# Performance work log

Hardware: AMD Instinct MI355X
Metric: run time of the kernel (lower is better)

The kernel has to match this reference:

```python
import jax, jax.numpy as jnp
import numpy as np

D_MODEL = 1024
N_HEAD = 16


def setup_inputs() -> dict:
    key = jax.random.key(0)
    ks = jax.random.split(key, 12)
    B, S, D = 4, 2048, D_MODEL
    scale = 1.0 / np.sqrt(D)
    inp = {
        "Q": jax.random.normal(ks[0], (B, S, D), jnp.float32),
        "K": jax.random.normal(ks[1], (B, S, D), jnp.float32),
        "V": jax.random.normal(ks[2], (B, S, D), jnp.float32),
        "Wq": jax.random.normal(ks[3], (D, D), jnp.float32) * scale,
        "bq": jax.random.normal(ks[4], (D,), jnp.float32) * scale,
        "Wk": jax.random.normal(ks[5], (D, D), jnp.float32) * scale,
        "bk": jax.random.normal(ks[6], (D,), jnp.float32) * scale,
        "Wv": jax.random.normal(ks[7], (D, D), jnp.float32) * scale,
        "bv": jax.random.normal(ks[8], (D,), jnp.float32) * scale,
        "Wo": jax.random.normal(ks[9], (D, D), jnp.float32) * scale,
        "bo": jax.random.normal(ks[10], (D,), jnp.float32) * scale,
    }
    return inp


def _split_heads(x, n_head):
    B, S, D = x.shape
    return x.reshape(B, S, n_head, D // n_head).transpose(0, 2, 1, 3)  # [B,H,S,dh]


def reference(Q, K, V, Wq, bq, Wk, bk, Wv, bv, Wo, bo):
    # torch Linear: x @ W.T + b
    q = _split_heads(Q @ Wq.T + bq, N_HEAD)
    k = _split_heads(K @ Wk.T + bk, N_HEAD)
    v = _split_heads(V @ Wv.T + bv, N_HEAD)
    d_k = k.shape[-1]
    score = jnp.einsum('bhqd,bhkd->bhqk', q, k) / jnp.sqrt(jnp.float32(d_k))
    attn = jax.nn.softmax(score, axis=-1)
    out = jnp.einsum('bhqk,bhkd->bhqd', attn, v)  # [B,H,S,dh]
    B, H, S, dh = out.shape
    out = out.transpose(0, 2, 1, 3).reshape(B, S, H * dh)
    return out @ Wo.T + bo
```

## Files before the change

kernel.cpp:

```cpp
#include <hip/hip_runtime.h>
#include <math.h>

#define D_MODEL 1024
#define N_HEAD  16
#define DH      64
#define SEQ     2048
#define BATCH   4
#define BH      (BATCH*N_HEAD)
#define MROWS   (BATCH*SEQ)

typedef __attribute__((ext_vector_type(8)))  short          s16x8;
typedef __attribute__((ext_vector_type(8)))  unsigned short u16x8;
typedef __attribute__((ext_vector_type(4)))  unsigned short u16x4;
typedef __attribute__((ext_vector_type(4)))  float          f32x4;
typedef __attribute__((ext_vector_type(16))) float          f32x16;
typedef __attribute__((ext_vector_type(4)))  unsigned int   u32x4;

#define QSCALE 0.18033688f

__device__ __forceinline__ unsigned short f2bf(float x) {
    unsigned int u = __float_as_uint(x);
    u += 0x7FFFu + ((u >> 16) & 1u);
    return (unsigned short)(u >> 16);
}

__device__ __forceinline__ unsigned int cvtpk_bf16(float lo, float hi) {
    unsigned int r;
    asm("v_cvt_pk_bf16_f32 %0, %1, %2" : "=v"(r) : "v"(lo), "v"(hi));
    return r;
}

__device__ __forceinline__ float exp2_asm(float x) {
    float r;
    asm("v_exp_f32 %0, %1" : "=v"(r) : "v"(x));
    return r;
}

__global__ __launch_bounds__(256) void conv_w4(const float* __restrict__ w0,
                                               const float* __restrict__ w1,
                                               const float* __restrict__ w2,
                                               const float* __restrict__ w3,
                                               unsigned short* __restrict__ o0,
                                               unsigned short* __restrict__ o1,
                                               unsigned short* __restrict__ o2,
                                               unsigned short* __restrict__ o3)
{
    const float* w; unsigned short* o;
    switch (blockIdx.y) {
        case 0:  w = w0; o = o0; break;
        case 1:  w = w1; o = o1; break;
        case 2:  w = w2; o = o2; break;
        default: w = w3; o = o3; break;
    }
    int i = blockIdx.x * 256 + threadIdx.x;
    const float4* p = (const float4*)w + (size_t)i * 2;
    float4 a = p[0], b = p[1];
    u16x8 v;
    v[0] = f2bf(a.x); v[1] = f2bf(a.y); v[2] = f2bf(a.z); v[3] = f2bf(a.w);
    v[4] = f2bf(b.x); v[5] = f2bf(b.y); v[6] = f2bf(b.z); v[7] = f2bf(b.w);
    *((u16x8*)o + i) = v;
}

template<int MODE, bool AF32>
__global__ __launch_bounds__(256) void gemm_bt(const void* __restrict__ Av,
                                               const unsigned short* __restrict__ W,
                                               const float* __restrict__ bias,
                                               unsigned short* __restrict__ outb,
                                               float* __restrict__ outf,
                                               float oscale)
{
    __shared__ short As[128 * 64];
    __shared__ short Bs[128 * 64];
    const int tid = threadIdx.x;
    const int w = tid >> 6, l = tid & 63;
    const int lr = l & 15, lg = l >> 4;
    const int wm = w >> 1, wn = w & 1;
    const int r0 = blockIdx.x * 128, c0 = blockIdx.y * 128;
    const int srow = tid >> 3;
    const int sc8  = tid & 7;

    f32x4 zz = {0.f, 0.f, 0.f, 0.f};
    f32x4 acc[4][4];
    #pragma unroll
    for (int i = 0; i < 4; ++i)
        #pragma unroll
        for (int j = 0; j < 4; ++j) acc[i][j] = zz;

    const unsigned short* Ab = (const unsigned short*)Av;
    const float*          Af = (const float*)Av;

    u16x8 ar[4], br[4];
    float4 arf[4][2];
    #pragma unroll
    for (int p = 0; p < 4; ++p) {
        int row = p * 32 + srow;
        if (AF32) {
            arf[p][0] = *(const float4*)(Af + (size_t)(r0 + row) * 1024 + sc8 * 8);
            arf[p][1] = *(const float4*)(Af + (size_t)(r0 + row) * 1024 + sc8 * 8 + 4);
        } else {
            ar[p] = *(const u16x8*)(Ab + (size_t)(r0 + row) * 1024 + sc8 * 8);
        }
        br[p] = *(const u16x8*)(W + (size_t)(c0 + row) * 1024 + sc8 * 8);
    }

    for (int ks = 0; ks < 16; ++ks) {
        __syncthreads();
        #pragma unroll
        for (int p = 0; p < 4; ++p) {
            int row = p * 32 + srow;
            if (AF32) {
                u32x4 wd;
                wd[0] = cvtpk_bf16(arf[p][0].x, arf[p][0].y);
                wd[1] = cvtpk_bf16(arf[p][0].z, arf[p][0].w);
                wd[2] = cvtpk_bf16(arf[p][1].x, arf[p][1].y);
                wd[3] = cvtpk_bf16(arf[p][1].z, arf[p][1].w);
                *(u16x8*)&As[row * 64 + ((sc8 ^ (row & 7)) * 8)] = __builtin_bit_cast(u16x8, wd);
            } else {
                *(u16x8*)&As[row * 64 + ((sc8 ^ (row & 7)) * 8)] = ar[p];
            }
            *(u16x8*)&Bs[row * 64 + ((sc8 ^ (row & 7)) * 8)] = br[p];
        }
        __syncthreads();
        if (ks < 15) {
            int k0 = (ks + 1) * 64;
            #pragma unroll
            for (int p = 0; p < 4; ++p) {
                int row = p * 32 + srow;
                if (AF32) {
                    arf[p][0] = *(const float4*)(Af + (size_t)(r0 + row) * 1024 + k0 + sc8 * 8);
                    arf[p][1] = *(const float4*)(Af + (size_t)(r0 + row) * 1024 + k0 + sc8 * 8 + 4);
                } else {
                    ar[p] = *(const u16x8*)(Ab + (size_t)(r0 + row) * 1024 + k0 + sc8 * 8);
                }
                br[p] = *(const u16x8*)(W + (size_t)(c0 + row) * 1024 + k0 + sc8 * 8);
            }
        }
        #pragma unroll
        for (int t = 0; t < 2; ++t) {
            const int k8 = lg + 4 * t;
            s16x8 af[4], bw[4];
            #pragma unroll
            for (int i = 0; i < 4; ++i) {
                int rowa = wm * 64 + i * 16 + lr;
                af[i] = *(const s16x8*)&As[rowa * 64 + ((k8 ^ (rowa & 7)) * 8)];
                int rowb = wn * 64 + i * 16 + lr;
                bw[i] = *(const s16x8*)&Bs[rowb * 64 + ((k8 ^ (rowb & 7)) * 8)];
            }
            #pragma unroll
            for (int i = 0; i < 4; ++i)
                #pragma unroll
                for (int j = 0; j < 4; ++j)
                    acc[i][j] = __builtin_amdgcn_mfma_f32_16x16x32_bf16(af[i], bw[j], acc[i][j], 0, 0, 0);
        }
    }

    #pragma unroll
    for (int i = 0; i < 4; ++i) {
        #pragma unroll
        for (int j = 0; j < 4; ++j) {
            const int colb = c0 + wn * 64 + j * 16 + lr;
            const float bv = bias[colb];
            if (MODE == 2) {
                const int row = r0 + wm * 64 + i * 16 + lg * 4;
                const int b = row >> 11, s = row & 2047;
                const int h = colb >> 6, d = colb & 63;
                u16x4 pv;
                pv[0] = f2bf((acc[i][j][0] + bv) * oscale);
                pv[1] = f2bf((acc[i][j][1] + bv) * oscale);
                pv[2] = f2bf((acc[i][j][2] + bv) * oscale);
                pv[3] = f2bf((acc[i][j][3] + bv) * oscale);
                *(u16x4*)(outb + ((size_t)(b * N_HEAD + h) * DH + d) * SEQ + s) = pv;
            } else {
                #pragma unroll
                for (int rg = 0; rg < 4; ++rg) {
                    const int row = r0 + wm * 64 + i * 16 + lg * 4 + rg;
                    const float v = acc[i][j][rg] + bv;
                    if (MODE == 0) {
                        outf[(size_t)row * D_MODEL + colb] = v;
                    } else {
                        const int b = row >> 11, s = row & 2047;
                        const int h = colb >> 6, d = colb & 63;
                        outb[((size_t)(b * N_HEAD + h) * SEQ + s) * DH + d] = f2bf(v * oscale);
                    }
                }
            }
        }
    }
}

__global__ __launch_bounds__(256) void flash_attn_mfma32(const unsigned short* __restrict__ qb,
                                                         const unsigned short* __restrict__ kb,
                                                         const unsigned short* __restrict__ vtb,
                                                         unsigned short* __restrict__ aob)
{
    __shared__ u16x8 Kt[512];
    __shared__ u16x8 Vt[512];

    const int tid = threadIdx.x;
    const int w = tid >> 6, l = tid & 63;
    const int q32 = l & 31;
    const int h = l >> 5;
    const int qt = blockIdx.x, bh = blockIdx.y;
    const unsigned short* qh = qb + (size_t)bh * SEQ * DH;
    const unsigned short* kh = kb + (size_t)bh * SEQ * DH;
    const unsigned short* vh = vtb + (size_t)bh * DH * SEQ;

    const int qrow = qt * 128 + w * 32 + q32;

    s16x8 qf[4];
    #pragma unroll
    for (int ks = 0; ks < 4; ++ks)
        qf[ks] = *(const s16x8*)(qh + (size_t)qrow * DH + ks * 16 + h * 8);

    f32x16 O[2];
    #pragma unroll
    for (int c = 0; c < 2; ++c)
        #pragma unroll
        for (int r = 0; r < 16; ++r) O[c][r] = 0.f;
    float m = -1e30f, lsum = 0.f;

    const int srow = tid >> 3;
    const int sc8  = tid & 7;

    u16x8 kreg[2], vreg[2];
    #pragma unroll
    for (int p = 0; p < 2; ++p) {
        int rr = p * 32 + srow;
        kreg[p] = *(const u16x8*)(kh + (size_t)rr * DH + sc8 * 8);
        vreg[p] = *(const u16x8*)(vh + (size_t)rr * SEQ + sc8 * 8);
    }

    for (int kv = 0; kv < SEQ / 64; ++kv) {
        __syncthreads();
        #pragma unroll
        for (int p = 0; p < 2; ++p) {
            int rr = p * 32 + srow;
            Kt[sc8 * 64 + (rr ^ sc8)] = kreg[p];
            Vt[sc8 * 64 + (rr ^ sc8)] = vreg[p];
        }
        __syncthreads();
        if (kv < SEQ / 64 - 1) {
            const int s0 = (kv + 1) * 64;
            #pragma unroll
            for (int p = 0; p < 2; ++p) {
                int rr = p * 32 + srow;
                kreg[p] = *(const u16x8*)(kh + (size_t)(s0 + rr) * DH + sc8 * 8);
                vreg[p] = *(const u16x8*)(vh + (size_t)rr * SEQ + s0 + sc8 * 8);
            }
        }

        f32x16 SC[2];
        #pragma unroll
        for (int c = 0; c < 2; ++c)
            #pragma unroll
            for (int r = 0; r < 16; ++r) SC[c][r] = 0.f;
        #pragma unroll
        for (int ks = 0; ks < 4; ++ks) {
            const int chunk = 2 * ks + h;
            #pragma unroll
            for (int c = 0; c < 2; ++c) {
                const int row = c * 32 + q32;
                s16x8 kf = __builtin_bit_cast(s16x8, Kt[chunk * 64 + (row ^ chunk)]);
                SC[c] = __builtin_amdgcn_mfma_f32_32x32x16_bf16(kf, qf[ks], SC[c], 0, 0, 0);
            }
        }

        float t0[8];
        #pragma unroll
        for (int r = 0; r < 8; ++r)
            t0[r] = fmaxf(fmaxf(SC[0][r], SC[0][r + 8]), fmaxf(SC[1][r], SC[1][r + 8]));
        #pragma unroll
        for (int d = 4; d; d >>= 1)
            #pragma unroll
            for (int r = 0; r < d; ++r) t0[r] = fmaxf(t0[r], t0[r + d]);
        float rm = fmaxf(t0[0], __shfl_xor(t0[0], 32, 64));

        if (!__all(rm - m <= 8.0f)) {
            const float nm = fmaxf(m, rm);
            const float fold = exp2_asm(m - nm);
            lsum *= fold;
            O[0] *= fold;
            O[1] *= fold;
            m = nm;
        }

        #pragma unroll
        for (int c = 0; c < 2; ++c)
            #pragma unroll
            for (int r = 0; r < 16; ++r)
                SC[c][r] = exp2_asm(SC[c][r] - m);

        float s0a[8];
        #pragma unroll
        for (int r = 0; r < 8; ++r)
            s0a[r] = (SC[0][r] + SC[0][r + 8]) + (SC[1][r] + SC[1][r + 8]);
        #pragma unroll
        for (int d = 4; d; d >>= 1)
            #pragma unroll
            for (int r = 0; r < d; ++r) s0a[r] += s0a[r + d];
        lsum += s0a[0] + __shfl_xor(s0a[0], 32, 64);

        s16x8 pa[4];
        #pragma unroll
        for (int s = 0; s < 4; ++s) {
            const int c = s >> 1, rb = (s & 1) * 8;
            unsigned int a0 = cvtpk_bf16(SC[c][rb + 0], SC[c][rb + 1]);
            unsigned int a1 = cvtpk_bf16(SC[c][rb + 2], SC[c][rb + 3]);
            unsigned int b0 = cvtpk_bf16(SC[c][rb + 4], SC[c][rb + 5]);
            unsigned int b1 = cvtpk_bf16(SC[c][rb + 6], SC[c][rb + 7]);
            unsigned int x0 = (unsigned int)__shfl_xor((int)a0, 32, 64);
            unsigned int x1 = (unsigned int)__shfl_xor((int)a1, 32, 64);
            unsigned int y0 = (unsigned int)__shfl_xor((int)b0, 32, 64);
            unsigned int y1 = (unsigned int)__shfl_xor((int)b1, 32, 64);
            u32x4 wd;
            wd[0] = h ? y0 : a0;
            wd[1] = h ? y1 : a1;
            wd[2] = h ? b0 : x0;
            wd[3] = h ? b1 : x1;
            pa[s] = __builtin_bit_cast(s16x8, wd);
        }

        #pragma unroll
        for (int s = 0; s < 4; ++s) {
            const int chunk = 2 * s + h;
            #pragma unroll
            for (int c = 0; c < 2; ++c) {
                const int row = c * 32 + q32;
                s16x8 vf = __builtin_bit_cast(s16x8, Vt[chunk * 64 + (row ^ chunk)]);
                O[c] = __builtin_amdgcn_mfma_f32_32x32x16_bf16(vf, pa[s], O[c], 0, 0, 0);
            }
        }
    }

    const float inv = 1.0f / lsum;
    const int b = bh >> 4, head = bh & 15;
    unsigned short* obase = aob + ((size_t)b * SEQ + qrow) * D_MODEL + head * DH;
    #pragma unroll
    for (int c = 0; c < 2; ++c) {
        #pragma unroll
        for (int rq = 0; rq < 4; ++rq) {
            const int d0 = 8 * rq + 4 * h + 32 * c;
            u16x4 pv;
            #pragma unroll
            for (int j = 0; j < 4; ++j) pv[j] = f2bf(O[c][rq * 4 + j] * inv);
            *(u16x4*)(obase + d0) = pv;
        }
    }
}

extern "C" void kernel_launch(void* const* d_in, const int* in_sizes, int n_in,
                              void* d_out, int out_size, void* d_ws, size_t ws_size,
                              hipStream_t stream)
{
    const float* Q  = (const float*)d_in[0];
    const float* K  = (const float*)d_in[1];
    const float* V  = (const float*)d_in[2];
    const float* Wq = (const float*)d_in[3];
    const float* bq = (const float*)d_in[4];
    const float* Wk = (const float*)d_in[5];
    const float* bk = (const float*)d_in[6];
    const float* Wv = (const float*)d_in[7];
    const float* bv = (const float*)d_in[8];
    const float* Wo = (const float*)d_in[9];
    const float* bo = (const float*)d_in[10];

    const size_t PER = (size_t)MROWS * D_MODEL;
    const size_t WSZ = (size_t)D_MODEL * D_MODEL;
    unsigned short* wqb = (unsigned short*)d_ws;
    unsigned short* wkb = wqb + WSZ;
    unsigned short* wvb = wkb + WSZ;
    unsigned short* wob = wvb + WSZ;
    unsigned short* qb2 = wob + WSZ;
    unsigned short* kb2 = qb2 + PER;
    unsigned short* vtb = kb2 + PER;
    unsigned short* aob = vtb + PER;

    dim3 gg(MROWS / 128, D_MODEL / 128);

    conv_w4<<<dim3(512, 4), 256, 0, stream>>>(Wq, Wk, Wv, Wo, wqb, wkb, wvb, wob);

    gemm_bt<1, true><<<gg, 256, 0, stream>>>(Q, wqb, bq, qb2, nullptr, QSCALE);
    gemm_bt<1, true><<<gg, 256, 0, stream>>>(K, wkb, bk, kb2, nullptr, 1.0f);
    gemm_bt<2, true><<<gg, 256, 0, stream>>>(V, wvb, bv, vtb, nullptr, 1.0f);

    flash_attn_mfma32<<<dim3(SEQ / 128, BH), 256, 0, stream>>>(qb2, kb2, vtb, aob);

    gemm_bt<0, false><<<gg, 256, 0, stream>>>(aob, wob, bo, nullptr, (float*)d_out, 1.0f);
}
```

Baseline: 245.5 us.

## Merge QKV GEMMs, double-buffer flash attention LDS, remap blocks per XCD

The three QKV projection GEMMs are merged into one launch that picks its operands from blockIdx.z, which cuts launch overhead and gives a larger grid. The flash attention kernel now double-buffers its K/V tiles in LDS, which removes one barrier per iteration. It also seeds the score accumulator with -m so the max subtraction comes for free. Further changes raise the MFMA issue priority with s_setprio, add a launch-bounds occupancy hint, and remap the 1D grid so that all query tiles of a head stay on the same XCD for L2 reuse. The costs are double the LDS use, and a running max that starts at 0 and is only rescaled when it exceeds a threshold, which could affect numerical robustness.

```diff
diff --git a/kernel.cpp b/kernel.cpp
--- a/kernel.cpp
+++ b/kernel.cpp
@@ -61,13 +61,132 @@
     *((u16x8*)o + i) = v;
 }
 
-template<int MODE, bool AF32>
-__global__ __launch_bounds__(256) void gemm_bt(const void* __restrict__ Av,
-                                               const unsigned short* __restrict__ W,
-                                               const float* __restrict__ bias,
-                                               unsigned short* __restrict__ outb,
-                                               float* __restrict__ outf,
-                                               float oscale)
+__global__ __launch_bounds__(256) void qkv_gemm(const float* __restrict__ Qi,
+                                                const float* __restrict__ Ki,
+                                                const float* __restrict__ Vi,
+                                                const unsigned short* __restrict__ wq,
+                                                const unsigned short* __restrict__ wk,
+                                                const unsigned short* __restrict__ wv,
+                                                const float* __restrict__ bqp,
+                                                const float* __restrict__ bkp,
+                                                const float* __restrict__ bvp,
+                                                unsigned short* __restrict__ qo,
+                                                unsigned short* __restrict__ ko,
+                                                unsigned short* __restrict__ vo)
+{
+    __shared__ short As[128 * 64];
+    __shared__ short Bs[128 * 64];
+
+    const float* Af; const unsigned short* W; const float* bias; unsigned short* outb;
+    switch (blockIdx.z) {
+        case 0:  Af = Qi; W = wq; bias = bqp; outb = qo; break;
+        case 1:  Af = Ki; W = wk; bias = bkp; outb = ko; break;
+        default: Af = Vi; W = wv; bias = bvp; outb = vo; break;
+    }
+    const float oscale = (blockIdx.z == 0) ? QSCALE : 1.0f;
+    const bool  tmode  = (blockIdx.z == 2);
+
+    const int tid = threadIdx.x;
+    const int w = tid >> 6, l = tid & 63;
+    const int lr = l & 15, lg = l >> 4;
+    const int wm = w >> 1, wn = w & 1;
+    const int r0 = blockIdx.x * 128, c0 = blockIdx.y * 128;
+    const int srow = tid >> 3;
+    const int sc8  = tid & 7;
+
+    f32x4 zz = {0.f, 0.f, 0.f, 0.f};
+    f32x4 acc[4][4];
+    #pragma unroll
+    for (int i = 0; i < 4; ++i)
+        #pragma unroll
+        for (int j = 0; j < 4; ++j) acc[i][j] = zz;
+
+    u16x8 br[4];
+    float4 arf[4][2];
+    #pragma unroll
+    for (int p = 0; p < 4; ++p) {
+        int row = p * 32 + srow;
+        arf[p][0] = *(const float4*)(Af + (size_t)(r0 + row) * 1024 + sc8 * 8);
+        arf[p][1] = *(const float4*)(Af + (size_t)(r0 + row) * 1024 + sc8 * 8 + 4);
+        br[p] = *(const u16x8*)(W + (size_t)(c0 + row) * 1024 + sc8 * 8);
+    }
+
+    for (int ks = 0; ks < 16; ++ks) {
+        __syncthreads();
+        #pragma unroll
+        for (int p = 0; p < 4; ++p) {
+            int row = p * 32 + srow;
+            u32x4 wd;
+            wd[0] = cvtpk_bf16(arf[p][0].x, arf[p][0].y);
+            wd[1] = cvtpk_bf16(arf[p][0].z, arf[p][0].w);
+            wd[2] = cvtpk_bf16(arf[p][1].x, arf[p][1].y);
+            wd[3] = cvtpk_bf16(arf[p][1].z, arf[p][1].w);
+            *(u16x8*)&As[row * 64 + ((sc8 ^ (row & 7)) * 8)] = __builtin_bit_cast(u16x8, wd);
+            *(u16x8*)&Bs[row * 64 + ((sc8 ^ (row & 7)) * 8)] = br[p];
+        }
+        __syncthreads();
+        if (ks < 15) {
+            int k0 = (ks + 1) * 64;
+            #pragma unroll
+            for (int p = 0; p < 4; ++p) {
+                int row = p * 32 + srow;
+                arf[p][0] = *(const float4*)(Af + (size_t)(r0 + row) * 1024 + k0 + sc8 * 8);
+                arf[p][1] = *(const float4*)(Af + (size_t)(r0 + row) * 1024 + k0 + sc8 * 8 + 4);
+                br[p] = *(const u16x8*)(W + (size_t)(c0 + row) * 1024 + k0 + sc8 * 8);
+            }
+        }
+        #pragma unroll
+        for (int t = 0; t < 2; ++t) {
+            const int k8 = lg + 4 * t;
+            s16x8 af[4], bw[4];
+            #pragma unroll
+            for (int i = 0; i < 4; ++i) {
+                int rowa = wm * 64 + i * 16 + lr;
+                af[i] = *(const s16x8*)&As[rowa * 64 + ((k8 ^ (rowa & 7)) * 8)];
+                int rowb = wn * 64 + i * 16 + lr;
+                bw[i] = *(const s16x8*)&Bs[rowb * 64 + ((k8 ^ (rowb & 7)) * 8)];
+            }
+            #pragma unroll
+            for (int i = 0; i < 4; ++i)
+                #pragma unroll
+                for (int j = 0; j < 4; ++j)
+                    acc[i][j] = __builtin_amdgcn_mfma_f32_16x16x32_bf16(af[i], bw[j], acc[i][j], 0, 0, 0);
+        }
+    }
+
+    #pragma unroll
+    for (int i = 0; i < 4; ++i) {
+        #pragma unroll
+        for (int j = 0; j < 4; ++j) {
+            const int colb = c0 + wn * 64 + j * 16 + lr;
+            const float bv = bias[colb];
+            const int hh = colb >> 6, dd = colb & 63;
+            if (tmode) {
+                const int row = r0 + wm * 64 + i * 16 + lg * 4;
+                const int b = row >> 11, s = row & 2047;
+                u16x4 pv;
+                pv[0] = f2bf(acc[i][j][0] + bv);
+                pv[1] = f2bf(acc[i][j][1] + bv);
+                pv[2] = f2bf(acc[i][j][2] + bv);
+                pv[3] = f2bf(acc[i][j][3] + bv);
+                *(u16x4*)(outb + ((size_t)(b * N_HEAD + hh) * DH + dd) * SEQ + s) = pv;
+            } else {
+                #pragma unroll
+                for (int rg = 0; rg < 4; ++rg) {
+                    const int row = r0 + wm * 64 + i * 16 + lg * 4 + rg;
+                    const int b = row >> 11, s = row & 2047;
+                    outb[((size_t)(b * N_HEAD + hh) * SEQ + s) * DH + dd] =
+                        f2bf((acc[i][j][rg] + bv) * oscale);
+                }
+            }
+        }
+    }
+}
+
+__global__ __launch_bounds__(256) void gemm_out(const unsigned short* __restrict__ A,
+                                                const unsigned short* __restrict__ W,
+                                                const float* __restrict__ bias,
+                                                float* __restrict__ outf)
 {
     __shared__ short As[128 * 64];
     __shared__ short Bs[128 * 64];
@@ -86,20 +205,11 @@
         #pragma unroll
         for (int j = 0; j < 4; ++j) acc[i][j] = zz;
 
-    const unsigned short* Ab = (const unsigned short*)Av;
-    const float*          Af = (const float*)Av;
-
     u16x8 ar[4], br[4];
-    float4 arf[4][2];
     #pragma unroll
     for (int p = 0; p < 4; ++p) {
         int row = p * 32 + srow;
-        if (AF32) {
-            arf[p][0] = *(const float4*)(Af + (size_t)(r0 + row) * 1024 + sc8 * 8);
-            arf[p][1] = *(const float4*)(Af + (size_t)(r0 + row) * 1024 + sc8 * 8 + 4);
-        } else {
-            ar[p] = *(const u16x8*)(Ab + (size_t)(r0 + row) * 1024 + sc8 * 8);
-        }
+        ar[p] = *(const u16x8*)(A + (size_t)(r0 + row) * 1024 + sc8 * 8);
         br[p] = *(const u16x8*)(W + (size_t)(c0 + row) * 1024 + sc8 * 8);
     }
 
@@ -108,16 +218,7 @@
         #pragma unroll
         for (int p = 0; p < 4; ++p) {
             int row = p * 32 + srow;
-            if (AF32) {
-                u32x4 wd;
-                wd[0] = cvtpk_bf16(arf[p][0].x, arf[p][0].y);
-                wd[1] = cvtpk_bf16(arf[p][0].z, arf[p][0].w);
-                wd[2] = cvtpk_bf16(arf[p][1].x, arf[p][1].y);
-                wd[3] = cvtpk_bf16(arf[p][1].z, arf[p][1].w);
-                *(u16x8*)&As[row * 64 + ((sc8 ^ (row & 7)) * 8)] = __builtin_bit_cast(u16x8, wd);
-            } else {
-                *(u16x8*)&As[row * 64 + ((sc8 ^ (row & 7)) * 8)] = ar[p];
-            }
+            *(u16x8*)&As[row * 64 + ((sc8 ^ (row & 7)) * 8)] = ar[p];
             *(u16x8*)&Bs[row * 64 + ((sc8 ^ (row & 7)) * 8)] = br[p];
         }
         __syncthreads();
@@ -126,12 +227,7 @@
             #pragma unroll
             for (int p = 0; p < 4; ++p) {
                 int row = p * 32 + srow;
-                if (AF32) {
-                    arf[p][0] = *(const float4*)(Af + (size_t)(r0 + row) * 1024 + k0 + sc8 * 8);
-                    arf[p][1] = *(const float4*)(Af + (size_t)(r0 + row) * 1024 + k0 + sc8 * 8 + 4);
-                } else {
-                    ar[p] = *(const u16x8*)(Ab + (size_t)(r0 + row) * 1024 + k0 + sc8 * 8);
-                }
+                ar[p] = *(const u16x8*)(A + (size_t)(r0 + row) * 1024 + k0 + sc8 * 8);
                 br[p] = *(const u16x8*)(W + (size_t)(c0 + row) * 1024 + k0 + sc8 * 8);
             }
         }
@@ -160,47 +256,34 @@
         for (int j = 0; j < 4; ++j) {
             const int colb = c0 + wn * 64 + j * 16 + lr;
             const float bv = bias[colb];
-            if (MODE == 2) {
-                const int row = r0 + wm * 64 + i * 16 + lg * 4;
-                const int b = row >> 11, s = row & 2047;
-                const int h = colb >> 6, d = colb & 63;
-                u16x4 pv;
-                pv[0] = f2bf((acc[i][j][0] + bv) * oscale);
-                pv[1] = f2bf((acc[i][j][1] + bv) * oscale);
-                pv[2] = f2bf((acc[i][j][2] + bv) * oscale);
-                pv[3] = f2bf((acc[i][j][3] + bv) * oscale);
-                *(u16x4*)(outb + ((size_t)(b * N_HEAD + h) * DH + d) * SEQ + s) = pv;
-            } else {
-                #pragma unroll
-                for (int rg = 0; rg < 4; ++rg) {
-                    const int row = r0 + wm * 64 + i * 16 + lg * 4 + rg;
-                    const float v = acc[i][j][rg] + bv;
-                    if (MODE == 0) {
-                        outf[(size_t)row * D_MODEL + colb] = v;
-                    } else {
-                        const int b = row >> 11, s = row & 2047;
-                        const int h = colb >> 6, d = colb & 63;
-                        outb[((size_t)(b * N_HEAD + h) * SEQ + s) * DH + d] = f2bf(v * oscale);
-                    }
-                }
-            }
-        }
-    }
-}
-
-__global__ __launch_bounds__(256) void flash_attn_mfma32(const unsigned short* __restrict__ qb,
-                                                         const unsigned short* __restrict__ kb,
-                                                         const unsigned short* __restrict__ vtb,
-                                                         unsigned short* __restrict__ aob)
+            #pragma unroll
+            for (int rg = 0; rg < 4; ++rg) {
+                const int row = r0 + wm * 64 + i * 16 + lg * 4 + rg;
+                outf[(size_t)row * D_MODEL + colb] = acc[i][j][rg] + bv;
+            }
+        }
+    }
+}
+
+__global__ __launch_bounds__(256, 4) void flash_attn_mfma32(const unsigned short* __restrict__ qb,
+                                                            const unsigned short* __restrict__ kb,
+                                                            const unsigned short* __restrict__ vtb,
+                                                            unsigned short* __restrict__ aob)
 {
-    __shared__ u16x8 Kt[512];
-    __shared__ u16x8 Vt[512];
+    __shared__ u16x8 Kt[2][512];
+    __shared__ u16x8 Vt[2][512];
 
     const int tid = threadIdx.x;
     const int w = tid >> 6, l = tid & 63;
     const int q32 = l & 31;
     const int h = l >> 5;
-    const int qt = blockIdx.x, bh = blockIdx.y;
+
+    const int wg   = blockIdx.x;
+    const int xcd  = wg & 7;
+    const int slot = wg >> 3;
+    const int bh   = xcd * 8 + (slot >> 4);
+    const int qt   = slot & 15;
+
     const unsigned short* qh = qb + (size_t)bh * SEQ * DH;
     const unsigned short* kh = kb + (size_t)bh * SEQ * DH;
     const unsigned short* vh = vtb + (size_t)bh * DH * SEQ;
@@ -217,7 +300,7 @@
     for (int c = 0; c < 2; ++c)
         #pragma unroll
         for (int r = 0; r < 16; ++r) O[c][r] = 0.f;
-    float m = -1e30f, lsum = 0.f;
+    float m = 0.f, lsum = 0.f;
 
     const int srow = tid >> 3;
     const int sc8  = tid & 7;
@@ -229,16 +312,16 @@
         kreg[p] = *(const u16x8*)(kh + (size_t)rr * DH + sc8 * 8);
         vreg[p] = *(const u16x8*)(vh + (size_t)rr * SEQ + sc8 * 8);
     }
-
+    #pragma unroll
+    for (int p = 0; p < 2; ++p) {
+        int rr = p * 32 + srow;
+        Kt[0][sc8 * 64 + (rr ^ sc8)] = kreg[p];
+        Vt[0][sc8 * 64 + (rr ^ sc8)] = vreg[p];
+    }
+    __syncthreads();
+
+    int buf = 0;
     for (int kv = 0; kv < SEQ / 64; ++kv) {
-        __syncthreads();
-        #pragma unroll
-        for (int p = 0; p < 2; ++p) {
-            int rr = p * 32 + srow;
-            Kt[sc8 * 64 + (rr ^ sc8)] = kreg[p];
-            Vt[sc8 * 64 + (rr ^ sc8)] = vreg[p];
-        }
-        __syncthreads();
         if (kv < SEQ / 64 - 1) {
             const int s0 = (kv + 1) * 64;
             #pragma unroll
@@ -249,46 +332,53 @@
             }
         }
 
+        f32x16 seed;
+        #pragma unroll
+        for (int r = 0; r < 16; ++r) seed[r] = -m;
         f32x16 SC[2];
-        #pragma unroll
-        for (int c = 0; c < 2; ++c)
-            #pragma unroll
-            for (int r = 0; r < 16; ++r) SC[c][r] = 0.f;
+        SC[0] = seed; SC[1] = seed;
+        __builtin_amdgcn_s_setprio(1);
         #pragma unroll
         for (int ks = 0; ks < 4; ++ks) {
             const int chunk = 2 * ks + h;
             #pragma unroll
             for (int c = 0; c < 2; ++c) {
                 const int row = c * 32 + q32;
-                s16x8 kf = __builtin_bit_cast(s16x8, Kt[chunk * 64 + (row ^ chunk)]);
+                s16x8 kf = __builtin_bit_cast(s16x8, Kt[buf][chunk * 64 + (row ^ chunk)]);
                 SC[c] = __builtin_amdgcn_mfma_f32_32x32x16_bf16(kf, qf[ks], SC[c], 0, 0, 0);
             }
         }
+        __builtin_amdgcn_s_setprio(0);
 
         float t0[8];
         #pragma unroll
         for (int r = 0; r < 8; ++r)
-            t0[r] = fmaxf(fmaxf(SC[0][r], SC[0][r + 8]), fmaxf(SC[1][r], SC[1][r + 8]));
+            t0[r] = fmaxf(fmaxf(fmaxf(SC[0][r], SC[0][r + 8]), SC[1][r]), SC[1][r + 8]);
         #pragma unroll
         for (int d = 4; d; d >>= 1)
             #pragma unroll
             for (int r = 0; r < d; ++r) t0[r] = fmaxf(t0[r], t0[r + d]);
-        float rm = fmaxf(t0[0], __shfl_xor(t0[0], 32, 64));
-
-        if (!__all(rm - m <= 8.0f)) {
-            const float nm = fmaxf(m, rm);
-            const float fold = exp2_asm(m - nm);
+        float rmb = fmaxf(t0[0], __shfl_xor(t0[0], 32, 64));
+
+        if (!__all(rmb <= 8.0f)) {
+            const float delta = fmaxf(rmb, 0.f);
+            const float fold = exp2_asm(-delta);
             lsum *= fold;
             O[0] *= fold;
             O[1] *= fold;
-            m = nm;
+            m += delta;
+            #pragma unroll
+            for (int c = 0; c < 2; ++c)
+                #pragma unroll
+                for (int r = 0; r < 16; ++r)
+                    SC[c][r] -= delta;
         }
 
         #pragma unroll
         for (int c = 0; c < 2; ++c)
             #pragma unroll
             for (int r = 0; r < 16; ++r)
-                SC[c][r] = exp2_asm(SC[c][r] - m);
+                SC[c][r] = exp2_asm(SC[c][r]);
 
         float s0a[8];
         #pragma unroll
@@ -320,15 +410,28 @@
             pa[s] = __builtin_bit_cast(s16x8, wd);
         }
 
+        __builtin_amdgcn_s_setprio(1);
         #pragma unroll
         for (int s = 0; s < 4; ++s) {
             const int chunk = 2 * s + h;
             #pragma unroll
             for (int c = 0; c < 2; ++c) {
                 const int row = c * 32 + q32;
-                s16x8 vf = __builtin_bit_cast(s16x8, Vt[chunk * 64 + (row ^ chunk)]);
+                s16x8 vf = __builtin_bit_cast(s16x8, Vt[buf][chunk * 64 + (row ^ chunk)]);
                 O[c] = __builtin_amdgcn_mfma_f32_32x32x16_bf16(vf, pa[s], O[c], 0, 0, 0);
             }
+        }
+        __builtin_amdgcn_s_setprio(0);
+
+        if (kv < SEQ / 64 - 1) {
+            #pragma unroll
+            for (int p = 0; p < 2; ++p) {
+                int rr = p * 32 + srow;
+                Kt[buf ^ 1][sc8 * 64 + (rr ^ sc8)] = kreg[p];
+                Vt[buf ^ 1][sc8 * 64 + (rr ^ sc8)] = vreg[p];
+            }
+            __syncthreads();
+            buf ^= 1;
         }
     }
 
@@ -375,15 +478,12 @@
     unsigned short* vtb = kb2 + PER;
     unsigned short* aob = vtb + PER;
 
-    dim3 gg(MROWS / 128, D_MODEL / 128);
-
     conv_w4<<<dim3(512, 4), 256, 0, stream>>>(Wq, Wk, Wv, Wo, wqb, wkb, wvb, wob);
 
-    gemm_bt<1, true><<<gg, 256, 0, stream>>>(Q, wqb, bq, qb2, nullptr, QSCALE);
-    gemm_bt<1, true><<<gg, 256, 0, stream>>>(K, wkb, bk, kb2, nullptr, 1.0f);
-    gemm_bt<2, true><<<gg, 256, 0, stream>>>(V, wvb, bv, vtb, nullptr, 1.0f);
-
-    flash_attn_mfma32<<<dim3(SEQ / 128, BH), 256, 0, stream>>>(qb2, kb2, vtb, aob);
-
-    gemm_bt<0, false><<<gg, 256, 0, stream>>>(aob, wob, bo, nullptr, (float*)d_out, 1.0f);
-}
+    qkv_gemm<<<dim3(MROWS / 128, D_MODEL / 128, 3), 256, 0, stream>>>(
+        Q, K, V, wqb, wkb, wvb, bq, bk, bv, qb2, kb2, vtb);
+
+    flash_attn_mfma32<<<dim3(16 * BH), 256, 0, stream>>>(qb2, kb2, vtb, aob);
+
+    gemm_out<<<dim3(MROWS / 128, D_MODEL / 128), 256, 0, stream>>>(aob, wob, bo, (float*)d_out);
+}
```

Measured after the change: 221.6 us. 1.11x faster.
